# Kernel optimization log

Measured on AMD Instinct MI355X. Metric: run time of the kernel, lower is better.

## Reference

```python
import jax, jax.numpy as jnp
import numpy as np

NEG = -1000000.0  # mask value used by the torch module


def setup_inputs() -> dict:
    key = jax.random.key(0)
    k1, k2, k3, k4 = jax.random.split(key, 4)
    B, Q, K, D = 16, 2048, 2048, 128
    queries = jax.random.normal(k1, (B, Q, D), dtype=jnp.float32)
    keys = jax.random.normal(k2, (B, K, D), dtype=jnp.float32)
    values = jax.random.normal(k3, (B, K, D), dtype=jnp.float32)
    valid_lens = jax.random.randint(k4, (B,), 0, K, dtype=jnp.int32)
    return {"queries": queries, "keys": keys, "values": values, "valid_lens": valid_lens}


def reference(queries, keys, values, valid_lens):
    d = queries.shape[-1]
    # scores: [B, Q, K]
    scores = jnp.einsum("bqd,bkd->bqk", queries, keys) / jnp.sqrt(jnp.float32(d))
    # mask key positions >= valid_len[b] with the same -1e6 value as torch
    kv_pos = jnp.arange(scores.shape[-1])  # [K]
    mask = kv_pos[None, None, :] < valid_lens[:, None, None]  # [B,1,K]
    scores = jnp.where(mask, scores, NEG)
    attn = jax.nn.softmax(scores, axis=-1)
    # dropout p=0.0 -> identity (module in eval)
    return jnp.einsum("bqk,bkd->bqd", attn, values)
```

## Files before the change

### kernel.cpp

```cpp
#include <hip/hip_runtime.h>
#include <hip/hip_bf16.h>

#define NB    16
#define NQ    2048
#define NKV   2048
#define DH    128
#define KVT   64
#define NTILE 32
#define TILE_BYTES 16384
#define TILE_ELT   8192

typedef __attribute__((ext_vector_type(8))) short short8;
typedef __attribute__((ext_vector_type(4))) float f32x4;

__device__ __forceinline__ unsigned short f2bf(float f) {
    union { float f; unsigned int u; } x; x.f = f;
    unsigned int r = (x.u + 0x7fffu + ((x.u >> 16) & 1u)) >> 16;
    return (unsigned short)r;
}

__device__ __forceinline__ void load_lds16(const void* g, void* l) {
    __builtin_amdgcn_global_load_lds(
        (const __attribute__((address_space(1))) unsigned int*)g,
        (__attribute__((address_space(3))) unsigned int*)l, 16, 0, 0);
}

__global__ __launch_bounds__(256)
void preconv(const float* __restrict__ kg, const float* __restrict__ vg,
             const int* __restrict__ vlg,
             unsigned short* __restrict__ kws, unsigned short* __restrict__ vws) {
    __shared__ __align__(16) unsigned short lv[TILE_ELT];
    const int tid = threadIdx.x;
    const int rb = (blockIdx.x & 7) * 64 + (blockIdx.x >> 3);
    const int b = rb >> 5, t = rb & 31;
    const int vl = vlg[b];
    const int ntiles = (vl == 0) ? NTILE : ((vl + KVT - 1) >> 6);
    if (t >= ntiles) return;

    const float* kb = kg + ((size_t)b * NKV + t * KVT) * DH;
    const float* vb = vg + ((size_t)b * NKV + t * KVT) * DH;
    char* kimg = (char*)(kws + (size_t)(b * NTILE + t) * TILE_ELT);
    char* vimg = (char*)(vws + (size_t)(b * NTILE + t) * TILE_ELT);

    #pragma unroll
    for (int p = 0; p < 4; ++p) {
        int idx = p * 256 + tid;
        int row = idx >> 4, ch = idx & 15;
        f32x4 a = *(const f32x4*)(kb + row * DH + ch * 8);
        f32x4 c = *(const f32x4*)(kb + row * DH + ch * 8 + 4);
        union { short8 v; unsigned short u[8]; } w;
        #pragma unroll
        for (int j = 0; j < 4; ++j) { w.u[j] = f2bf(a[j]); w.u[4 + j] = f2bf(c[j]); }
        *(short8*)(kimg + row * 256 + ((ch * 16) ^ ((row & 7) << 4))) = w.v;
        f32x4 va = *(const f32x4*)(vb + row * DH + ch * 8);
        f32x4 vc = *(const f32x4*)(vb + row * DH + ch * 8 + 4);
        union { short8 v; unsigned short u[8]; } w2;
        #pragma unroll
        for (int j = 0; j < 4; ++j) { w2.u[j] = f2bf(va[j]); w2.u[4 + j] = f2bf(vc[j]); }
        *(short8*)((char*)lv + row * 256 + ((ch * 16) ^ (((row >> 3) & 7) << 4))) = w2.v;
    }
    __syncthreads();
    #pragma unroll
    for (int p = 0; p < 4; ++p) {
        int task = p * 256 + tid;
        int c = task & 7, d = task >> 3;
        union { short8 v; unsigned short u[8]; } w;
        #pragma unroll
        for (int j = 0; j < 8; ++j) {
            int kv = c * 8 + j;
            w.u[j] = *(const unsigned short*)((const char*)lv + kv * 256 + ((d * 2) ^ (((kv >> 3) & 7) << 4)));
        }
        *(short8*)(vimg + d * 128 + ((c * 16) ^ ((d & 7) << 4))) = w.v;
    }
}

__global__ __launch_bounds__(128, 2)
void attn_fwd3(const float* __restrict__ qg,
               const unsigned short* __restrict__ kws,
               const unsigned short* __restrict__ vws,
               const int* __restrict__ vlg, float* __restrict__ og) {
    __shared__ __align__(16) unsigned short lds_k[TILE_ELT];
    __shared__ __align__(16) unsigned short lds_v[TILE_ELT];
    __shared__ __align__(16) unsigned short lds_p[2][16 * KVT];

    const int tid = threadIdx.x;
    const int lane = tid & 63;
    const int wv = tid >> 6;
    const int row16 = lane & 15;
    const int g = lane >> 4;

    const int bid = blockIdx.x;
    const int b  = bid & 15;
    const int qt = bid >> 4;
    const int q0 = qt * 32 + wv * 16;
    const int vl = vlg[b];

    const float QS = 1.4426950408889634f * 0.08838834764831845f;
    short8 qf[4];
    {
        const float* qp = qg + ((size_t)b * NQ + q0 + row16) * DH + g * 8;
        #pragma unroll
        for (int c = 0; c < 4; ++c) {
            f32x4 a  = *(const f32x4*)(qp + c * 32);
            f32x4 bb = *(const f32x4*)(qp + c * 32 + 4);
            union { short8 v; unsigned short u[8]; } t;
            #pragma unroll
            for (int j = 0; j < 4; ++j) { t.u[j] = f2bf(a[j] * QS); t.u[4 + j] = f2bf(bb[j] * QS); }
            qf[c] = t.v;
        }
    }

    const int ntiles = (vl == 0) ? NTILE : ((vl + KVT - 1) >> 6);
    const float MASKV = (vl == 0) ? 0.0f : -1442695.0f;

    f32x4 oacc[8];
    f32x4 ellacc = (f32x4){0.f, 0.f, 0.f, 0.f};
    #pragma unroll
    for (int n = 0; n < 8; ++n) oacc[n] = (f32x4){0.f, 0.f, 0.f, 0.f};
    short8 ones;
    {
        union { short8 v; unsigned short u[8]; } t;
        #pragma unroll
        for (int j = 0; j < 8; ++j) t.u[j] = 0x3F80;
        ones = t.v;
    }

    const char* kbase = (const char*)kws + (size_t)b * NTILE * TILE_BYTES;
    const char* vbase = (const char*)vws + (size_t)b * NTILE * TILE_BYTES;

    for (int tt = 0; tt < ntiles; ++tt) {
        __syncthreads();
        const char* ks = kbase + (size_t)tt * TILE_BYTES;
        const char* vs = vbase + (size_t)tt * TILE_BYTES;
        #pragma unroll
        for (int i = 0; i < 8; ++i) {
            int off = i * 2048 + wv * 1024;
            load_lds16(ks + off + lane * 16, (char*)lds_k + off);
            load_lds16(vs + off + lane * 16, (char*)lds_v + off);
        }
        asm volatile("s_waitcnt vmcnt(0)" ::: "memory");
        __syncthreads();

        f32x4 s[4];
        __builtin_amdgcn_s_setprio(1);
        #pragma unroll
        for (int n = 0; n < 4; ++n) {
            s[n] = (f32x4){0.f, 0.f, 0.f, 0.f};
            int krow = n * 16 + row16;
            #pragma unroll
            for (int c = 0; c < 4; ++c) {
                short8 kf = *(const short8*)((const char*)lds_k + krow * 256 +
                                             ((c * 64 + g * 16) ^ ((krow & 7) << 4)));
                s[n] = __builtin_amdgcn_mfma_f32_16x16x32_bf16(qf[c], kf, s[n], 0, 0, 0);
            }
        }
        __builtin_amdgcn_s_setprio(0);

        if (vl == 0 || tt == ntiles - 1) {
            int kvb = tt * KVT;
            #pragma unroll
            for (int n = 0; n < 4; ++n) {
                if (kvb + n * 16 + row16 >= vl) {
                    #pragma unroll
                    for (int r = 0; r < 4; ++r) s[n][r] = MASKV;
                }
            }
        }

        #pragma unroll
        for (int n = 0; n < 4; ++n) {
            #pragma unroll
            for (int r = 0; r < 4; ++r) {
                float p = __builtin_amdgcn_exp2f(s[n][r]);
                int qr = g * 4 + r;
                int swz = (g ^ (r << 1)) & 7;
                __hip_bfloat16 h = __float2bfloat16(p);
                *(unsigned short*)((char*)lds_p[wv] + qr * 128 +
                                   (((n * 16 + row16) * 2) ^ (swz << 4))) =
                    *reinterpret_cast<unsigned short*>(&h);
            }
        }
        asm volatile("s_waitcnt lgkmcnt(0)" ::: "memory");

        const int swzr = ((row16 >> 2) ^ ((row16 & 3) << 1)) & 7;
        __builtin_amdgcn_s_setprio(1);
        #pragma unroll
        for (int kc = 0; kc < 2; ++kc) {
            short8 pf = *(const short8*)((const char*)lds_p[wv] + row16 * 128 +
                                         ((kc * 64 + g * 16) ^ (swzr << 4)));
            ellacc = __builtin_amdgcn_mfma_f32_16x16x32_bf16(pf, ones, ellacc, 0, 0, 0);
            #pragma unroll
            for (int n2 = 0; n2 < 8; ++n2) {
                int vrow = n2 * 16 + row16;
                short8 vf = *(const short8*)((const char*)lds_v + vrow * 128 +
                                             ((kc * 64 + g * 16) ^ ((vrow & 7) << 4)));
                oacc[n2] = __builtin_amdgcn_mfma_f32_16x16x32_bf16(pf, vf, oacc[n2], 0, 0, 0);
            }
        }
        __builtin_amdgcn_s_setprio(0);
    }

    float* ob = og + ((size_t)b * NQ + q0) * DH;
    float rl[4];
    #pragma unroll
    for (int r = 0; r < 4; ++r) rl[r] = 1.0f / ellacc[r];
    #pragma unroll
    for (int n2 = 0; n2 < 8; ++n2) {
        #pragma unroll
        for (int r = 0; r < 4; ++r)
            ob[(size_t)(g * 4 + r) * DH + n2 * 16 + row16] = oacc[n2][r] * rl[r];
    }
}

extern "C" void kernel_launch(void* const* d_in, const int* in_sizes, int n_in,
                              void* d_out, int out_size, void* d_ws, size_t ws_size,
                              hipStream_t stream) {
    const float* q  = (const float*)d_in[0];
    const float* k  = (const float*)d_in[1];
    const float* v  = (const float*)d_in[2];
    const int*   vl = (const int*)d_in[3];
    float* o = (float*)d_out;

    unsigned short* kws = (unsigned short*)d_ws;
    unsigned short* vws = (unsigned short*)((char*)d_ws + (size_t)NB * NTILE * TILE_BYTES);
    preconv<<<dim3(NB * NTILE), dim3(256), 0, stream>>>(k, v, vl, kws, vws);
    attn_fwd3<<<dim3(NB * 64), dim3(128), 0, stream>>>(q, kws, vws, vl, o);
}
```

Measured before the change: 69.90 us.

## Split KV tiles across blocks with partial outputs and a combine kernel

Turns the attention kernel into a split-KV form. Each block now has 4 waves covering 64 query rows and handles an interleaved subset of KV tiles, with S chosen from the workspace size. Partial unnormalized outputs and row sums go to the workspace, and a new combine kernel sums and normalizes them. K fragment loads are also batched ahead of the MFMAs. This is meant to balance work across batches with uneven valid lengths and raise parallelism, at the cost of extra partial-output traffic and a third launch.

```diff
diff --git a/kernel.cpp b/kernel.cpp
--- a/kernel.cpp
+++ b/kernel.cpp
@@ -74,14 +74,18 @@
     }
 }
 
-__global__ __launch_bounds__(128, 2)
-void attn_fwd3(const float* __restrict__ qg,
-               const unsigned short* __restrict__ kws,
-               const unsigned short* __restrict__ vws,
-               const int* __restrict__ vlg, float* __restrict__ og) {
+__global__ __launch_bounds__(256, 4)
+void attn_split(const float* __restrict__ qg,
+                const unsigned short* __restrict__ kws,
+                const unsigned short* __restrict__ vws,
+                const int* __restrict__ vlg,
+                float* __restrict__ og,
+                float* __restrict__ opart,
+                float* __restrict__ ellg,
+                int S) {
     __shared__ __align__(16) unsigned short lds_k[TILE_ELT];
     __shared__ __align__(16) unsigned short lds_v[TILE_ELT];
-    __shared__ __align__(16) unsigned short lds_p[2][16 * KVT];
+    __shared__ __align__(16) unsigned short lds_p[4][16 * KVT];
 
     const int tid = threadIdx.x;
     const int lane = tid & 63;
@@ -90,10 +94,20 @@
     const int g = lane >> 4;
 
     const int bid = blockIdx.x;
-    const int b  = bid & 15;
-    const int qt = bid >> 4;
-    const int q0 = qt * 32 + wv * 16;
+    const int b    = bid & 15;
+    const int rest = bid >> 4;
+    const int qt   = rest & 31;
+    const int s    = rest >> 5;
+    const int q0   = qt * 64 + wv * 16;
     const int vl = vlg[b];
+
+    const int nt = (vl == 0) ? NTILE : ((vl + KVT - 1) >> 6);
+
+    if (s >= nt) {
+        if (tid < 64)
+            ellg[(size_t)s * NB * NQ + (size_t)b * NQ + qt * 64 + tid] = 0.f;
+        return;
+    }
 
     const float QS = 1.4426950408889634f * 0.08838834764831845f;
     short8 qf[4];
@@ -110,7 +124,6 @@
         }
     }
 
-    const int ntiles = (vl == 0) ? NTILE : ((vl + KVT - 1) >> 6);
     const float MASKV = (vl == 0) ? 0.0f : -1442695.0f;
 
     f32x4 oacc[8];
@@ -127,51 +140,55 @@
 
     const char* kbase = (const char*)kws + (size_t)b * NTILE * TILE_BYTES;
     const char* vbase = (const char*)vws + (size_t)b * NTILE * TILE_BYTES;
-
-    for (int tt = 0; tt < ntiles; ++tt) {
-        __syncthreads();
+    const int swzr = ((row16 >> 2) ^ ((row16 & 3) << 1)) & 7;
+
+    for (int tt = s; tt < nt; tt += S) {
         const char* ks = kbase + (size_t)tt * TILE_BYTES;
         const char* vs = vbase + (size_t)tt * TILE_BYTES;
         #pragma unroll
-        for (int i = 0; i < 8; ++i) {
-            int off = i * 2048 + wv * 1024;
+        for (int i = 0; i < 4; ++i) {
+            int off = i * 4096 + wv * 1024;
             load_lds16(ks + off + lane * 16, (char*)lds_k + off);
             load_lds16(vs + off + lane * 16, (char*)lds_v + off);
         }
         asm volatile("s_waitcnt vmcnt(0)" ::: "memory");
         __syncthreads();
 
-        f32x4 s[4];
+        f32x4 sc[4];
+        #pragma unroll
+        for (int n = 0; n < 4; ++n) sc[n] = (f32x4){0.f, 0.f, 0.f, 0.f};
         __builtin_amdgcn_s_setprio(1);
         #pragma unroll
-        for (int n = 0; n < 4; ++n) {
-            s[n] = (f32x4){0.f, 0.f, 0.f, 0.f};
-            int krow = n * 16 + row16;
-            #pragma unroll
-            for (int c = 0; c < 4; ++c) {
-                short8 kf = *(const short8*)((const char*)lds_k + krow * 256 +
-                                             ((c * 64 + g * 16) ^ ((krow & 7) << 4)));
-                s[n] = __builtin_amdgcn_mfma_f32_16x16x32_bf16(qf[c], kf, s[n], 0, 0, 0);
-            }
+        for (int c = 0; c < 4; ++c) {
+            short8 kf[4];
+            #pragma unroll
+            for (int n = 0; n < 4; ++n) {
+                int krow = n * 16 + row16;
+                kf[n] = *(const short8*)((const char*)lds_k + krow * 256 +
+                                         ((c * 64 + g * 16) ^ ((krow & 7) << 4)));
+            }
+            #pragma unroll
+            for (int n = 0; n < 4; ++n)
+                sc[n] = __builtin_amdgcn_mfma_f32_16x16x32_bf16(qf[c], kf[n], sc[n], 0, 0, 0);
         }
         __builtin_amdgcn_s_setprio(0);
 
-        if (vl == 0 || tt == ntiles - 1) {
+        if (vl == 0 || tt == nt - 1) {
             int kvb = tt * KVT;
             #pragma unroll
             for (int n = 0; n < 4; ++n) {
                 if (kvb + n * 16 + row16 >= vl) {
                     #pragma unroll
-                    for (int r = 0; r < 4; ++r) s[n][r] = MASKV;
+                    for (int r = 0; r < 4; ++r) sc[n][r] = MASKV;
                 }
             }
         }
 
         #pragma unroll
-        for (int n = 0; n < 4; ++n) {
+        for (int n = 0; n < 4; ++n)
             #pragma unroll
             for (int r = 0; r < 4; ++r) {
-                float p = __builtin_amdgcn_exp2f(s[n][r]);
+                float p = __builtin_amdgcn_exp2f(sc[n][r]);
                 int qr = g * 4 + r;
                 int swz = (g ^ (r << 1)) & 7;
                 __hip_bfloat16 h = __float2bfloat16(p);
@@ -179,10 +196,8 @@
                                    (((n * 16 + row16) * 2) ^ (swz << 4))) =
                     *reinterpret_cast<unsigned short*>(&h);
             }
-        }
         asm volatile("s_waitcnt lgkmcnt(0)" ::: "memory");
 
-        const int swzr = ((row16 >> 2) ^ ((row16 & 3) << 1)) & 7;
         __builtin_amdgcn_s_setprio(1);
         #pragma unroll
         for (int kc = 0; kc < 2; ++kc) {
@@ -198,18 +213,52 @@
             }
         }
         __builtin_amdgcn_s_setprio(0);
-    }
-
-    float* ob = og + ((size_t)b * NQ + q0) * DH;
-    float rl[4];
-    #pragma unroll
-    for (int r = 0; r < 4; ++r) rl[r] = 1.0f / ellacc[r];
-    #pragma unroll
-    for (int n2 = 0; n2 < 8; ++n2) {
-        #pragma unroll
-        for (int r = 0; r < 4; ++r)
-            ob[(size_t)(g * 4 + r) * DH + n2 * 16 + row16] = oacc[n2][r] * rl[r];
-    }
+
+        __syncthreads();
+    }
+
+    if (S == 1) {
+        float* ob = og + ((size_t)b * NQ + q0) * DH;
+        float rl[4];
+        #pragma unroll
+        for (int r = 0; r < 4; ++r) rl[r] = 1.0f / ellacc[r];
+        #pragma unroll
+        for (int n2 = 0; n2 < 8; ++n2)
+            #pragma unroll
+            for (int r = 0; r < 4; ++r)
+                ob[(size_t)(g * 4 + r) * DH + n2 * 16 + row16] = oacc[n2][r] * rl[r];
+    } else {
+        float* op = opart + ((size_t)s * NB * NQ + (size_t)b * NQ + q0) * DH;
+        #pragma unroll
+        for (int n2 = 0; n2 < 8; ++n2)
+            #pragma unroll
+            for (int r = 0; r < 4; ++r)
+                op[(size_t)(g * 4 + r) * DH + n2 * 16 + row16] = oacc[n2][r];
+        if (row16 == 0) {
+            float* el = ellg + (size_t)s * NB * NQ + (size_t)b * NQ + q0;
+            #pragma unroll
+            for (int r = 0; r < 4; ++r) el[g * 4 + r] = ellacc[r];
+        }
+    }
+}
+
+__global__ __launch_bounds__(256)
+void combine(const float* __restrict__ opart, const float* __restrict__ ellg,
+             float* __restrict__ og, int S) {
+    int idx = blockIdx.x * 256 + threadIdx.x;
+    int row = idx >> 5;
+    int c   = idx & 31;
+    f32x4 acc = (f32x4){0.f, 0.f, 0.f, 0.f};
+    float l = 0.f;
+    for (int s = 0; s < S; ++s) {
+        float le = ellg[(size_t)s * NB * NQ + row];
+        if (le != 0.f) {
+            acc += ((const f32x4*)opart)[((size_t)s * NB * NQ + row) * 32 + c];
+            l += le;
+        }
+    }
+    float rl = 1.0f / l;
+    ((f32x4*)og)[(size_t)row * 32 + c] = acc * rl;
 }
 
 extern "C" void kernel_launch(void* const* d_in, const int* in_sizes, int n_in,
@@ -221,8 +270,23 @@
     const int*   vl = (const int*)d_in[3];
     float* o = (float*)d_out;
 
+    const size_t IMG = (size_t)NB * NTILE * TILE_BYTES;
+    const size_t ELL_OFF = 2 * IMG;
+    const size_t ELL_MAX = (size_t)4 * NB * NQ * 4;
+    const size_t OP_OFF  = ELL_OFF + ELL_MAX;
+    const size_t OP_ONE  = (size_t)NB * NQ * DH * 4;
+
+    int S = 1;
+    if (ws_size >= OP_OFF + 4 * OP_ONE) S = 4;
+    else if (ws_size >= OP_OFF + 2 * OP_ONE) S = 2;
+
     unsigned short* kws = (unsigned short*)d_ws;
-    unsigned short* vws = (unsigned short*)((char*)d_ws + (size_t)NB * NTILE * TILE_BYTES);
+    unsigned short* vws = (unsigned short*)((char*)d_ws + IMG);
+    float* ellg  = (float*)((char*)d_ws + ELL_OFF);
+    float* opart = (float*)((char*)d_ws + OP_OFF);
+
     preconv<<<dim3(NB * NTILE), dim3(256), 0, stream>>>(k, v, vl, kws, vws);
-    attn_fwd3<<<dim3(NB * 64), dim3(128), 0, stream>>>(q, kws, vws, vl, o);
-}
+    attn_split<<<dim3(NB * 32 * S), dim3(256), 0, stream>>>(q, kws, vws, vl, o, opart, ellg, S);
+    if (S > 1)
+        combine<<<dim3(NB * NQ * 32 / 256), dim3(256), 0, stream>>>(opart, ellg, o, S);
+}
```

Measured after the change: 76.12 us. +8.9%, slower.
